# Kernel optimization log

Measured on AMD Instinct MI355X. Metric: run time of the kernel, lower is better.

Reference implementation:

```python
import jax, jax.numpy as jnp
import numpy as np

NV = 6890   # SMPL vertex count (hard-coded in module)
NF = 13776  # SMPL face count
BATCH = 64


def _make_laplacian():
    # Mirrors LaplacianLoss.__init__: symmetric -1 adjacency from triangle
    # faces, diagonal = vertex degree, each row normalized by diag + 1e-8.
    rng = np.random.default_rng(0)
    faces = rng.integers(0, NV, size=(NF, 3))
    L = np.zeros((NV, NV), dtype=np.float32)
    L[faces[:, 0], faces[:, 1]] = -1
    L[faces[:, 1], faces[:, 0]] = -1
    L[faces[:, 1], faces[:, 2]] = -1
    L[faces[:, 2], faces[:, 1]] = -1
    L[faces[:, 2], faces[:, 0]] = -1
    L[faces[:, 0], faces[:, 2]] = -1
    r, c = np.diag_indices(NV)
    L[r, c] = -L.sum(1)
    L = L / (np.diag(L)[:, None] + 1e-8)
    return jnp.asarray(L)


def setup_inputs() -> dict:
    key = jax.random.key(0)
    x = jax.random.normal(key, (BATCH, NV, 3), dtype=jnp.float32)
    laplacian = _make_laplacian()
    return {"x": x, "laplacian": laplacian}


def reference(x, laplacian):
    # Dense Laplacian applied per batch: [v,w] x [b,w,d] -> [b,v,d]
    lx = jnp.einsum('vw,bwd->bvd', laplacian, x)
    # Squared norm over coordinate dim, then mean over (batch, vertices)
    # (average=False branch of the original module).
    return jnp.mean(jnp.sum(lx * lx, axis=2))
```

## Files before the change

kernel.cpp:

```cpp
#include <hip/hip_runtime.h>

#define NV    6890
#define NB    64
#define NCOL  192
#define CAP_W 512
#define MAIN4 1722
#define SCALE (1.0f / (64.0f * 6890.0f))

__global__ __launch_bounds__(256) void transpose_x_kernel(
    const float* __restrict__ x, float* __restrict__ Xt) {
  int i = blockIdx.x * blockDim.x + threadIdx.x;
  const int total = NB * NV * 3;
  if (i >= total) return;
  int d = i % 3;
  int w = (i / 3) % NV;
  int b = i / (3 * NV);
  Xt[(size_t)w * NCOL + b * 3 + d] = x[i];
}

template <bool USE_XT, bool USE_PARTIALS>
__global__ __launch_bounds__(256) void lap_rows_wave_kernel(
    const float* __restrict__ L,
    const float* __restrict__ X,
    float* __restrict__ partials,
    float* __restrict__ out_atomic) {
  const int lane = threadIdx.x & 63;
  const int wv   = threadIdx.x >> 6;
  const int v    = blockIdx.x * 4 + wv;
  if (v >= NV) return;

  __shared__ float s_val[4][CAP_W];
  __shared__ int   s_idx[4][CAP_W];
  float* __restrict__ sval = s_val[wv];
  int*   __restrict__ sidx = s_idx[wv];

  const float* __restrict__ row = L + (size_t)v * NV;
  const int head     = (v & 1) ? 2 : 0;
  const int extraPos = head ? 0 : (NV - 2);
  const float4* __restrict__ m4 = (const float4*)(row + head);

  const unsigned long long lmask = (1ull << lane) - 1ull;

  const int n0 = lane, n1 = lane + 64, n2 = lane + 128;
  const size_t o0 = (size_t)(n0 / 3) * (NV * 3) + (n0 % 3);
  const size_t o1 = (size_t)(n1 / 3) * (NV * 3) + (n1 % 3);
  const size_t o2 = (size_t)(n2 / 3) * (NV * 3) + (n2 % 3);

  float a0 = 0.f, a1 = 0.f, a2 = 0.f;
  int nnz = 0;

  auto apply = [&](int count) {
    for (int j = 0; j < count; ++j) {
      float val = sval[j];
      int   col = sidx[j];
      if (USE_XT) {
        const float* __restrict__ xr = X + (size_t)col * NCOL;
        a0 = fmaf(val, xr[n0], a0);
        a1 = fmaf(val, xr[n1], a1);
        a2 = fmaf(val, xr[n2], a2);
      } else {
        const size_t cb = (size_t)col * 3;
        a0 = fmaf(val, X[cb + o0], a0);
        a1 = fmaf(val, X[cb + o1], a1);
        a2 = fmaf(val, X[cb + o2], a2);
      }
    }
  };

  auto push = [&](bool nz, float val, int col) {
    unsigned long long m = __ballot(nz);
    if (nz) {
      int pos = nnz + __popcll(m & lmask);
      sval[pos] = val;
      sidx[pos] = col;
    }
    nnz += __popcll(m);
  };

  {
    const bool act = lane < 2;
    const int  col = extraPos + lane;
    float val = act ? row[col] : 0.f;
    push(act && val != 0.f, val, col);
  }

  for (int it = 0; it < 27; ++it) {
    const int i = it * 64 + lane;
    const bool act = i < MAIN4;
    float4 f = make_float4(0.f, 0.f, 0.f, 0.f);
    if (act) f = m4[i];
    const int cb = head + i * 4;
    push(act && f.x != 0.f, f.x, cb);
    push(act && f.y != 0.f, f.y, cb + 1);
    push(act && f.z != 0.f, f.z, cb + 2);
    push(act && f.w != 0.f, f.w, cb + 3);
    if (nnz > CAP_W - 260) { apply(nnz); nnz = 0; }
  }
  apply(nnz);

  float sq = fmaf(a0, a0, fmaf(a1, a1, a2 * a2));
  #pragma unroll
  for (int o = 32; o > 0; o >>= 1) sq += __shfl_down(sq, o);
  if (lane == 0) {
    if (USE_PARTIALS) partials[v] = sq;
    else              atomicAdd(out_atomic, sq * SCALE);
  }
}

__global__ __launch_bounds__(256) void reduce_kernel(
    const float* __restrict__ p, float* __restrict__ out) {
  int tid = threadIdx.x;
  float a = 0.0f;
  for (int i = tid; i < NV; i += 256) a += p[i];
  #pragma unroll
  for (int o = 32; o > 0; o >>= 1) a += __shfl_down(a, o);
  __shared__ float s_w[4];
  if ((tid & 63) == 0) s_w[tid >> 6] = a;
  __syncthreads();
  if (tid == 0) out[0] = (s_w[0] + s_w[1] + s_w[2] + s_w[3]) * SCALE;
}

__global__ void zero_out_kernel(float* p) {
  if (threadIdx.x == 0 && blockIdx.x == 0) p[0] = 0.0f;
}

extern "C" void kernel_launch(void* const* d_in, const int* in_sizes, int n_in,
                              void* d_out, int out_size, void* d_ws, size_t ws_size,
                              hipStream_t stream) {
  const float* x = (const float*)d_in[0];
  const float* L = (const float*)d_in[1];
  float* out = (float*)d_out;

  const size_t xt_bytes   = (size_t)NV * NCOL * sizeof(float);
  const size_t part_bytes = (size_t)NV * sizeof(float);
  const int grid = (NV + 3) / 4;

  if (ws_size >= xt_bytes + part_bytes) {
    float* Xt       = (float*)d_ws;
    float* partials = (float*)((char*)d_ws + xt_bytes);
    const int total = NB * NV * 3;
    transpose_x_kernel<<<(total + 255) / 256, 256, 0, stream>>>(x, Xt);
    lap_rows_wave_kernel<true, true><<<grid, 256, 0, stream>>>(L, Xt, partials, nullptr);
    reduce_kernel<<<1, 256, 0, stream>>>(partials, out);
  } else if (ws_size >= part_bytes) {
    float* partials = (float*)d_ws;
    lap_rows_wave_kernel<false, true><<<grid, 256, 0, stream>>>(L, x, partials, nullptr);
    reduce_kernel<<<1, 256, 0, stream>>>(partials, out);
  } else {
    zero_out_kernel<<<1, 64, 0, stream>>>(out);
    lap_rows_wave_kernel<false, false><<<grid, 256, 0, stream>>>(L, x, nullptr, out);
  }
}
```

Before: 57.00 us.

## Prefetch Laplacian rows, vectorize Xt gathers, and compact nonzeros once per row

The row scan now software-pipelines the float4 loads of the dense Laplacian row through a 4-deep register buffer. Nonzeros are compacted into one packed float2 shared-memory list (capacity 640) and applied once at the end, with a ballot/readlane fallback if a row overflows. The gather from the transposed X uses float4 loads on 48 lanes instead of three scalar loads per lane. The transpose kernel now writes coalesced and reads strided. The cost is more shared memory per block and a slow fallback path for dense rows.

Result: no change. 58.12 us (+2.0%).

```diff
diff --git a/kernel.cpp b/kernel.cpp
--- a/kernel.cpp
+++ b/kernel.cpp
@@ -3,19 +3,20 @@
 #define NV    6890
 #define NB    64
 #define NCOL  192
-#define CAP_W 512
+#define NC4   48
 #define MAIN4 1722
+#define NITP  28
+#define VCAP  640
 #define SCALE (1.0f / (64.0f * 6890.0f))
 
 __global__ __launch_bounds__(256) void transpose_x_kernel(
     const float* __restrict__ x, float* __restrict__ Xt) {
   int i = blockIdx.x * blockDim.x + threadIdx.x;
-  const int total = NB * NV * 3;
+  const int total = NV * NCOL;
   if (i >= total) return;
-  int d = i % 3;
-  int w = (i / 3) % NV;
-  int b = i / (3 * NV);
-  Xt[(size_t)w * NCOL + b * 3 + d] = x[i];
+  int n = i % NCOL;
+  int w = i / NCOL;
+  Xt[i] = x[(size_t)(n / 3) * (NV * 3) + (size_t)w * 3 + (n % 3)];
 }
 
 template <bool USE_XT, bool USE_PARTIALS>
@@ -29,16 +30,13 @@
   const int v    = blockIdx.x * 4 + wv;
   if (v >= NV) return;
 
-  __shared__ float s_val[4][CAP_W];
-  __shared__ int   s_idx[4][CAP_W];
-  float* __restrict__ sval = s_val[wv];
-  int*   __restrict__ sidx = s_idx[wv];
+  __shared__ float2 s_ent[4][VCAP];
+  float2* __restrict__ se = s_ent[wv];
 
   const float* __restrict__ row = L + (size_t)v * NV;
   const int head     = (v & 1) ? 2 : 0;
   const int extraPos = head ? 0 : (NV - 2);
   const float4* __restrict__ m4 = (const float4*)(row + head);
-
   const unsigned long long lmask = (1ull << lane) - 1ull;
 
   const int n0 = lane, n1 = lane + 64, n2 = lane + 128;
@@ -46,59 +44,95 @@
   const size_t o1 = (size_t)(n1 / 3) * (NV * 3) + (n1 % 3);
   const size_t o2 = (size_t)(n2 / 3) * (NV * 3) + (n2 % 3);
 
-  float a0 = 0.f, a1 = 0.f, a2 = 0.f;
-  int nnz = 0;
+  float4 acc = make_float4(0.f, 0.f, 0.f, 0.f);
 
-  auto apply = [&](int count) {
-    for (int j = 0; j < count; ++j) {
-      float val = sval[j];
-      int   col = sidx[j];
-      if (USE_XT) {
-        const float* __restrict__ xr = X + (size_t)col * NCOL;
-        a0 = fmaf(val, xr[n0], a0);
-        a1 = fmaf(val, xr[n1], a1);
-        a2 = fmaf(val, xr[n2], a2);
-      } else {
-        const size_t cb = (size_t)col * 3;
-        a0 = fmaf(val, X[cb + o0], a0);
-        a1 = fmaf(val, X[cb + o1], a1);
-        a2 = fmaf(val, X[cb + o2], a2);
+  auto gather = [&](float val, int col) {
+    if (USE_XT) {
+      if (lane < NC4) {
+        const float4 g = ((const float4*)X)[(size_t)col * NC4 + lane];
+        acc.x = fmaf(val, g.x, acc.x);
+        acc.y = fmaf(val, g.y, acc.y);
+        acc.z = fmaf(val, g.z, acc.z);
+        acc.w = fmaf(val, g.w, acc.w);
       }
+    } else {
+      const size_t cb = (size_t)col * 3;
+      acc.x = fmaf(val, X[cb + o0], acc.x);
+      acc.y = fmaf(val, X[cb + o1], acc.y);
+      acc.z = fmaf(val, X[cb + o2], acc.z);
     }
   };
 
+  int nnz = 0;
   auto push = [&](bool nz, float val, int col) {
     unsigned long long m = __ballot(nz);
-    if (nz) {
-      int pos = nnz + __popcll(m & lmask);
-      sval[pos] = val;
-      sidx[pos] = col;
-    }
+    int pos = nnz + __popcll(m & lmask);
+    if (nz && pos < VCAP) se[pos] = make_float2(val, __int_as_float(col));
     nnz += __popcll(m);
   };
 
+  float4 buf[4];
+  #pragma unroll
+  for (int k = 0; k < 4; ++k) buf[k] = m4[k * 64 + lane];
+
   {
     const bool act = lane < 2;
-    const int  col = extraPos + lane;
-    float val = act ? row[col] : 0.f;
-    push(act && val != 0.f, val, col);
+    const float val = act ? row[extraPos + lane] : 0.f;
+    push(act && val != 0.f, val, extraPos + lane);
   }
 
-  for (int it = 0; it < 27; ++it) {
+  #pragma unroll 4
+  for (int it = 0; it < NITP; ++it) {
+    const float4 f = buf[it & 3];
     const int i = it * 64 + lane;
+    buf[it & 3] = m4[min((it + 4) * 64 + lane, MAIN4 - 1)];
     const bool act = i < MAIN4;
-    float4 f = make_float4(0.f, 0.f, 0.f, 0.f);
-    if (act) f = m4[i];
     const int cb = head + i * 4;
     push(act && f.x != 0.f, f.x, cb);
     push(act && f.y != 0.f, f.y, cb + 1);
     push(act && f.z != 0.f, f.z, cb + 2);
     push(act && f.w != 0.f, f.w, cb + 3);
-    if (nnz > CAP_W - 260) { apply(nnz); nnz = 0; }
   }
-  apply(nnz);
 
-  float sq = fmaf(a0, a0, fmaf(a1, a1, a2 * a2));
+  if (nnz <= VCAP) {
+    const int cnt = nnz;
+    #pragma unroll 4
+    for (int j = 0; j < cnt; ++j) {
+      const float2 e = se[j];
+      gather(e.x, __float_as_int(e.y));
+    }
+  } else {
+    acc = make_float4(0.f, 0.f, 0.f, 0.f);
+    auto walk = [&](unsigned long long m, float src, int col0, int stride) {
+      while (m) {
+        const int s = (int)__builtin_ctzll(m);
+        m &= m - 1;
+        const float val =
+            __int_as_float(__builtin_amdgcn_readlane(__float_as_int(src), s));
+        gather(val, col0 + s * stride);
+      }
+    };
+    {
+      const bool act = lane < 2;
+      const float val = act ? row[extraPos + lane] : 0.f;
+      walk(__ballot(act && val != 0.f), val, extraPos, 1);
+    }
+    for (int it = 0; it < 27; ++it) {
+      const int i = it * 64 + lane;
+      const bool act = i < MAIN4;
+      float4 f = make_float4(0.f, 0.f, 0.f, 0.f);
+      if (act) f = m4[i];
+      const int cb = head + it * 256;
+      walk(__ballot(act && f.x != 0.f), f.x, cb + 0, 4);
+      walk(__ballot(act && f.y != 0.f), f.y, cb + 1, 4);
+      walk(__ballot(act && f.z != 0.f), f.z, cb + 2, 4);
+      walk(__ballot(act && f.w != 0.f), f.w, cb + 3, 4);
+    }
+  }
+
+  float sq = fmaf(acc.x, acc.x,
+             fmaf(acc.y, acc.y,
+             fmaf(acc.z, acc.z, acc.w * acc.w)));
   #pragma unroll
   for (int o = 32; o > 0; o >>= 1) sq += __shfl_down(sq, o);
   if (lane == 0) {
@@ -138,7 +172,7 @@
   if (ws_size >= xt_bytes + part_bytes) {
     float* Xt       = (float*)d_ws;
     float* partials = (float*)((char*)d_ws + xt_bytes);
-    const int total = NB * NV * 3;
+    const int total = NV * NCOL;
     transpose_x_kernel<<<(total + 255) / 256, 256, 0, stream>>>(x, Xt);
     lap_rows_wave_kernel<true, true><<<grid, 256, 0, stream>>>(L, Xt, partials, nullptr);
     reduce_kernel<<<1, 256, 0, stream>>>(partials, out);
```
